# Kernel tuning notes

Measured on AMD Instinct MI355X. Metric: run time of the kernel, lower is better.

## Reference

```python
import jax, jax.numpy as jnp
from jax import lax
import numpy as np

B, T, IN, H, NC, NL = 128, 256, 64, 256, 1, 2


def _lstm_dir(x, w_ih, w_hh, b_ih, b_hh, reverse):
    """Single-direction LSTM over x:[B,T,in]. PyTorch gate order i,f,g,o."""
    Bd = x.shape[0]
    Hd = w_hh.shape[1]
    # precompute input contribution to gates: [T,B,4H]
    xg = jnp.einsum('bti,gi->tbg', x, w_ih) + b_ih + b_hh

    def step(carry, xg_t):
        h, c = carry
        g = xg_t + h @ w_hh.T                      # [B,4H]
        i, f, gg, o = jnp.split(g, 4, axis=-1)
        i = jax.nn.sigmoid(i)
        f = jax.nn.sigmoid(f)
        gg = jnp.tanh(gg)
        o = jax.nn.sigmoid(o)
        c = f * c + i * gg
        h = o * jnp.tanh(c)
        return (h, c), h

    h0 = jnp.zeros((Bd, Hd), x.dtype)
    _, hs = lax.scan(step, (h0, h0), xg, reverse=reverse)
    return jnp.swapaxes(hs, 0, 1)                  # [B,T,H], time-aligned


def _bilstm(x, params):
    out = x
    for l in range(NL):
        fwd = _lstm_dir(out, params[f'w_ih_l{l}f'], params[f'w_hh_l{l}f'],
                        params[f'b_ih_l{l}f'], params[f'b_hh_l{l}f'], reverse=False)
        bwd = _lstm_dir(out, params[f'w_ih_l{l}b'], params[f'w_hh_l{l}b'],
                        params[f'b_ih_l{l}b'], params[f'b_hh_l{l}b'], reverse=True)
        out = jnp.concatenate([fwd, bwd], axis=-1)  # [B,T,2H]
        # (nn.LSTM dropout=0.2 is train-only between layers; eval -> identity)
    return out


def setup_inputs() -> dict:
    key = jax.random.key(0)
    ks = iter(jax.random.split(key, 32))
    inp = {'x': jax.random.normal(next(ks), (B, T, IN), jnp.float32)}
    s = 1.0 / np.sqrt(H)
    for l in range(NL):
        isz = IN if l == 0 else 2 * H
        for d in ('f', 'b'):
            inp[f'w_ih_l{l}{d}'] = jax.random.uniform(next(ks), (4 * H, isz), jnp.float32, -s, s)
            inp[f'w_hh_l{l}{d}'] = jax.random.uniform(next(ks), (4 * H, H), jnp.float32, -s, s)
            inp[f'b_ih_l{l}{d}'] = jax.random.uniform(next(ks), (4 * H,), jnp.float32, -s, s)
            inp[f'b_hh_l{l}{d}'] = jax.random.uniform(next(ks), (4 * H,), jnp.float32, -s, s)
    inp['fc_w'] = jax.random.uniform(next(ks), (NC, 2 * H), jnp.float32, -s, s)
    inp['fc_b'] = jax.random.uniform(next(ks), (NC,), jnp.float32, -s, s)
    return inp


def reference(x,
              w_ih_l0f, w_hh_l0f, b_ih_l0f, b_hh_l0f,
              w_ih_l0b, w_hh_l0b, b_ih_l0b, b_hh_l0b,
              w_ih_l1f, w_hh_l1f, b_ih_l1f, b_hh_l1f,
              w_ih_l1b, w_hh_l1b, b_ih_l1b, b_hh_l1b,
              fc_w, fc_b):
    params = dict(w_ih_l0f=w_ih_l0f, w_hh_l0f=w_hh_l0f, b_ih_l0f=b_ih_l0f, b_hh_l0f=b_hh_l0f,
                  w_ih_l0b=w_ih_l0b, w_hh_l0b=w_hh_l0b, b_ih_l0b=b_ih_l0b, b_hh_l0b=b_hh_l0b,
                  w_ih_l1f=w_ih_l1f, w_hh_l1f=w_hh_l1f, b_ih_l1f=b_ih_l1f, b_hh_l1f=b_hh_l1f,
                  w_ih_l1b=w_ih_l1b, w_hh_l1b=w_hh_l1b, b_ih_l1b=b_ih_l1b, b_hh_l1b=b_hh_l1b)
    out = _bilstm(x, params)          # [B,T,2H]
    last = out[:, -1, :]              # [B,2H]
    return last @ fc_w.T + fc_b       # [B,NC]
```

## Files before the change

kernel.cpp:

```cpp
#include <hip/hip_runtime.h>


typedef unsigned long long ull;

constexpr int B_ = 128, T_ = 256, IN_ = 64, H_ = 256;
constexpr int JW = 64;

#define KEEP_REG(x) asm volatile("" : "+v"(x))

__device__ __forceinline__ float sigmoid_(float x) { return 1.f / (1.f + __expf(-x)); }
__device__ __forceinline__ float tanh_(float x)    { return 1.f - 2.f / (1.f + __expf(2.f * x)); }
__device__ __forceinline__ int hidx(int k) { return (k >> 6) * 68 + (k & 63); }
__device__ __forceinline__ int widx(int gp, int jl, int ks, int kp) {
  return ((gp * 64 + jl) * 4 + ks) * 68 + kp;
}

template<int BB, bool L0M>
__global__ __launch_bounds__(256, 1)
void recur(const float* __restrict__ whh_f, const float* __restrict__ whh_b,
           const float* __restrict__ wih_f, const float* __restrict__ wih_b,
           const float* __restrict__ bih_f, const float* __restrict__ bhh_f,
           const float* __restrict__ bih_b, const float* __restrict__ bhh_b,
           const float* __restrict__ x,
           const float* __restrict__ xg,
           float* __restrict__ out0,
           float* __restrict__ hstate, float* __restrict__ cstate,
           float* __restrict__ hfinal,
           ull* __restrict__ ring,
           int ngroup, int dir_base, int nsteps, int step_base,
           int first, int save, int lastW)
{
  const int bid = blockIdx.x;
  const int kw  = bid & 3;
  const int gr  = (bid >> 2) % ngroup;
  const int dl  = (bid >> 2) / ngroup;
  const int d   = dir_base + dl;
  const int tid = threadIdx.x;
  const int jl  = tid >> 2;
  const int ks  = tid & 3;
  const int j   = kw * JW + jl;
  const int bbase = gr * BB;
  const int gidx  = dl * ngroup + gr;

  const float* whh  = d ? whh_b : whh_f;
  const float* wihp = d ? wih_b : wih_f;

  float wr[2][64];
  #pragma unroll
  for (int g = 0; g < 2; ++g) {
    const float* wrow = whh + (long)(g * H_ + j) * H_ + ks * 64;
    #pragma unroll
    for (int q = 0; q < 16; ++q) {
      const float4 w4 = *(const float4*)(wrow + q * 4);
      wr[g][q*4+0] = w4.x; wr[g][q*4+1] = w4.y;
      wr[g][q*4+2] = w4.z; wr[g][q*4+3] = w4.w;
    }
  }
  #pragma unroll
  for (int g = 0; g < 2; ++g)
    #pragma unroll
    for (int q = 0; q < 64; ++q) KEEP_REG(wr[g][q]);

  __shared__ alignas(16) float wlds[2 * 64 * 4 * 68];
  __shared__ alignas(16) float hbuf[2][BB][272];
  __shared__ alignas(16) float xt[2][4][64];
  #pragma unroll
  for (int gp = 0; gp < 2; ++gp) {
    const float* wrow = whh + (long)((gp + 2) * H_ + j) * H_ + ks * 64;
    float* dst = &wlds[widx(gp, jl, ks, 0)];
    #pragma unroll
    for (int q = 0; q < 16; ++q)
      *(float4*)(dst + q * 4) = *(const float4*)(wrow + q * 4);
  }

  float br[4];
  if constexpr (L0M) {
    const float* bih = d ? bih_b : bih_f;
    const float* bhh = d ? bhh_b : bhh_f;
    #pragma unroll
    for (int g = 0; g < 4; ++g) br[g] = bih[g * H_ + j] + bhh[g * H_ + j];
  }

  for (int idx = tid; idx < BB * H_; idx += 256) {
    const int b = idx >> 8, k = idx & 255;
    hbuf[0][b][hidx(k)] = first ? 0.f : hstate[(long)(bbase + b) * H_ + k];
  }
  float cs[BB];
  #pragma unroll
  for (int b = 0; b < BB; ++b)
    cs[b] = first ? 0.f : cstate[(long)(bbase + b) * H_ + j];

  if constexpr (L0M) {
    const int b = tid >> 6, kx = tid & 63;
    const int t0 = d ? T_ - 1 : 0;
    xt[0][b][kx] = x[((long)(bbase + b) * T_ + t0) * IN_ + kx];
  }
  float xr[BB][4], xn[BB][4];
  if constexpr (!L0M) {
    #pragma unroll
    for (int b = 0; b < BB; ++b)
      #pragma unroll
      for (int g = 0; g < 4; ++g)
        xr[b][g] = xg[(long)(bbase + b) * 1024 + g * H_ + j];
  }
  __syncthreads();

  const long ringstride = (long)2 * BB * H_;

  for (int s = 0; s < nsteps; ++s) {
    const int p = s & 1, wp = p ^ 1;
    const int gstep = step_base + s;

    float xpre = 0.f;
    if constexpr (L0M) {
      if (s + 1 < nsteps) {
        const int b = tid >> 6, kx = tid & 63;
        const int ttn = d ? (T_ - 2 - s) : (s + 1);
        xpre = x[((long)(bbase + b) * T_ + ttn) * IN_ + kx];
      }
    } else {
      const int sn = (s + 1 < nsteps) ? s + 1 : s;
      #pragma unroll
      for (int b = 0; b < BB; ++b)
        #pragma unroll
        for (int g = 0; g < 4; ++g)
          xn[b][g] = xg[((long)sn * B_ + bbase + b) * 1024 + g * H_ + j];
    }

    float acc[BB][4];
    #pragma unroll
    for (int b = 0; b < BB; ++b)
      #pragma unroll
      for (int g = 0; g < 4; ++g) acc[b][g] = 0.f;

    if constexpr (L0M) {
      #pragma unroll
      for (int gp = 0; gp < 2; ++gp) {
        const int g0 = 2 * gp, g1 = 2 * gp + 1;
        const float* wa = wihp + (long)(g0 * H_ + j) * IN_ + ks * 16;
        const float* wb = wihp + (long)(g1 * H_ + j) * IN_ + ks * 16;
        float4 wa_[4], wb_[4];
        #pragma unroll
        for (int q = 0; q < 4; ++q) { wa_[q] = *(const float4*)(wa + q * 4);
                                      wb_[q] = *(const float4*)(wb + q * 4); }
        #pragma unroll
        for (int b = 0; b < BB; ++b) {
          #pragma unroll
          for (int q = 0; q < 4; ++q) {
            const float4 xv = *(const float4*)&xt[p][b][ks * 16 + q * 4];
            acc[b][g0] = fmaf(xv.x, wa_[q].x, acc[b][g0]);
            acc[b][g0] = fmaf(xv.y, wa_[q].y, acc[b][g0]);
            acc[b][g0] = fmaf(xv.z, wa_[q].z, acc[b][g0]);
            acc[b][g0] = fmaf(xv.w, wa_[q].w, acc[b][g0]);
            acc[b][g1] = fmaf(xv.x, wb_[q].x, acc[b][g1]);
            acc[b][g1] = fmaf(xv.y, wb_[q].y, acc[b][g1]);
            acc[b][g1] = fmaf(xv.z, wb_[q].z, acc[b][g1]);
            acc[b][g1] = fmaf(xv.w, wb_[q].w, acc[b][g1]);
          }
        }
      }
      if (s + 1 < nsteps) {
        const int b = tid >> 6, kx = tid & 63;
        xt[wp][b][kx] = xpre;
      }
    }

    if (s > 0) {
      const unsigned want = (unsigned)gstep;
      ull* rg = ring + gidx * ringstride + (long)((gstep - 1) & 1) * (BB * H_);
      constexpr int NP = 3 * JW * BB;
      constexpr int NL = (NP + 255) / 256;
      ull vv[NL];
      #pragma unroll
      for (int q = 0; q < NL; ++q) {
        const int pidx = tid + q * 256;
        if (pidx < NP) {
          const int psl = pidx / (JW * BB), rem = pidx % (JW * BB);
          const int kwp = psl + (psl >= kw ? 1 : 0);
          vv[q] = __hip_atomic_load(rg + (rem >> 6) * H_ + kwp * JW + (rem & 63),
                                    __ATOMIC_RELAXED, __HIP_MEMORY_SCOPE_AGENT);
        }
      }
      long gd = 0;
      for (;;) {
        bool ok = true;
        #pragma unroll
        for (int q = 0; q < NL; ++q)
          if (tid + q * 256 < NP && (unsigned)(vv[q] >> 32) != want) ok = false;
        if (ok) break;
        if (++gd > (1L << 20)) break;
        __builtin_amdgcn_s_sleep(1);
        #pragma unroll
        for (int q = 0; q < NL; ++q) {
          const int pidx = tid + q * 256;
          if (pidx < NP && (unsigned)(vv[q] >> 32) != want) {
            const int psl = pidx / (JW * BB), rem = pidx % (JW * BB);
            const int kwp = psl + (psl >= kw ? 1 : 0);
            vv[q] = __hip_atomic_load(rg + (rem >> 6) * H_ + kwp * JW + (rem & 63),
                                      __ATOMIC_RELAXED, __HIP_MEMORY_SCOPE_AGENT);
          }
        }
      }
      #pragma unroll
      for (int q = 0; q < NL; ++q) {
        const int pidx = tid + q * 256;
        if (pidx < NP) {
          const int psl = pidx / (JW * BB), rem = pidx % (JW * BB);
          const int kwp = psl + (psl >= kw ? 1 : 0);
          hbuf[p][rem >> 6][hidx(kwp * JW + (rem & 63))] =
              __uint_as_float((unsigned)vv[q]);
        }
      }
    }
    __syncthreads();

    #pragma unroll
    for (int q = 0; q < 16; ++q) {
      const float4 wg = *(const float4*)&wlds[widx(0, jl, ks, q * 4)];
      const float4 wo = *(const float4*)&wlds[widx(1, jl, ks, q * 4)];
      #pragma unroll
      for (int b = 0; b < BB; ++b) {
        const float4 hv = *(const float4*)&hbuf[p][b][ks * 68 + q * 4];
        acc[b][0] = fmaf(hv.x, wr[0][q*4+0], acc[b][0]);
        acc[b][0] = fmaf(hv.y, wr[0][q*4+1], acc[b][0]);
        acc[b][0] = fmaf(hv.z, wr[0][q*4+2], acc[b][0]);
        acc[b][0] = fmaf(hv.w, wr[0][q*4+3], acc[b][0]);
        acc[b][1] = fmaf(hv.x, wr[1][q*4+0], acc[b][1]);
        acc[b][1] = fmaf(hv.y, wr[1][q*4+1], acc[b][1]);
        acc[b][1] = fmaf(hv.z, wr[1][q*4+2], acc[b][1]);
        acc[b][1] = fmaf(hv.w, wr[1][q*4+3], acc[b][1]);
        acc[b][2] = fmaf(hv.x, wg.x, acc[b][2]);
        acc[b][2] = fmaf(hv.y, wg.y, acc[b][2]);
        acc[b][2] = fmaf(hv.z, wg.z, acc[b][2]);
        acc[b][2] = fmaf(hv.w, wg.w, acc[b][2]);
        acc[b][3] = fmaf(hv.x, wo.x, acc[b][3]);
        acc[b][3] = fmaf(hv.y, wo.y, acc[b][3]);
        acc[b][3] = fmaf(hv.z, wo.z, acc[b][3]);
        acc[b][3] = fmaf(hv.w, wo.w, acc[b][3]);
      }
    }

    float hv_[BB];
    #pragma unroll
    for (int b = 0; b < BB; ++b) {
      #pragma unroll
      for (int g = 0; g < 4; ++g) {
        float a = acc[b][g];
        a += __shfl_xor(a, 1, 64);
        a += __shfl_xor(a, 2, 64);
        if constexpr (L0M) acc[b][g] = a + br[g];
        else               acc[b][g] = a + xr[b][g];
      }
      const float ig = sigmoid_(acc[b][0]);
      const float fg = sigmoid_(acc[b][1]);
      const float gg = tanh_(acc[b][2]);
      const float og = sigmoid_(acc[b][3]);
      cs[b] = fg * cs[b] + ig * gg;
      hv_[b] = og * tanh_(cs[b]);
    }

    if (ks < BB) {
      float hmine = hv_[0], cmine = cs[0];
      #pragma unroll
      for (int b = 1; b < BB; ++b)
        if (ks == b) { hmine = hv_[b]; cmine = cs[b]; }

      if (s < nsteps - 1) {
        const ull pv = ((ull)(unsigned)(gstep + 1) << 32) | (unsigned)__float_as_uint(hmine);
        __hip_atomic_store(ring + gidx * ringstride + (long)(gstep & 1) * (BB * H_)
                               + ks * H_ + j,
                           pv, __ATOMIC_RELAXED, __HIP_MEMORY_SCOPE_AGENT);
      }
      hbuf[wp][ks][hidx(j)] = hmine;

      if constexpr (L0M) {
        const int tt = d ? (T_ - 1 - gstep) : gstep;
        out0[((long)tt * B_ + bbase + ks) * 512 + d * H_ + j] = hmine;
      } else {
        if (s == nsteps - 1 && lastW)
          hfinal[(long)(bbase + ks) * 512 + (d ? H_ : 0) + j] = hmine;
      }
      if (save && s == nsteps - 1) {
        hstate[(long)(bbase + ks) * H_ + j] = hmine;
        cstate[(long)(bbase + ks) * H_ + j] = cmine;
      }
    }

    if constexpr (!L0M) {
      #pragma unroll
      for (int b = 0; b < BB; ++b)
        #pragma unroll
        for (int g = 0; g < 4; ++g) xr[b][g] = xn[b][g];
    }
  }
}

__global__ __launch_bounds__(256, 2)
void xg_gemm(const float* __restrict__ A, const float* __restrict__ W,
             const float* __restrict__ b1, const float* __restrict__ b2,
             float* __restrict__ C)
{
  __shared__ float As[16][128];
  __shared__ float Bs[16][132];
  const int tid = threadIdx.x;
  const int tx = tid & 15, ty = tid >> 4;
  const long m0 = (long)blockIdx.x * 128;
  const int  n0 = blockIdx.y * 128;
  const int sr = tid >> 1;
  const int sk = (tid & 1) * 8;
  const float* Ar = A + (m0 + sr) * 512 + sk;
  const float* Wr = W + (long)(n0 + sr) * 512 + sk;
  float acc[8][8];
  #pragma unroll
  for (int i = 0; i < 8; ++i)
    #pragma unroll
    for (int jj = 0; jj < 8; ++jj) acc[i][jj] = 0.f;

// ... 56 lines not shown
  const float* wp = fc_w + q * 128;
  #pragma unroll 4
  for (int k = 0; k < 128; ++k) s += hp[k] * wp[k];
  s += __shfl_xor(s, 1, 64);
  s += __shfl_xor(s, 2, 64);
  if (q == 0) out[b] = s + fc_b[0];
}

extern "C" void kernel_launch(void* const* d_in, const int* in_sizes, int n_in,
                              void* d_out, int out_size, void* d_ws, size_t ws_size,
                              hipStream_t stream)
{
  const float* x     = (const float*)d_in[0];
  const float* wih0f = (const float*)d_in[1];
  const float* whh0f = (const float*)d_in[2];
  const float* bih0f = (const float*)d_in[3];
  const float* bhh0f = (const float*)d_in[4];
  const float* wih0b = (const float*)d_in[5];
  const float* whh0b = (const float*)d_in[6];
  const float* bih0b = (const float*)d_in[7];
  const float* bhh0b = (const float*)d_in[8];
  const float* wih1f = (const float*)d_in[9];
  const float* whh1f = (const float*)d_in[10];
  const float* bih1f = (const float*)d_in[11];
  const float* bhh1f = (const float*)d_in[12];
  const float* wih1b = (const float*)d_in[13];
  const float* whh1b = (const float*)d_in[14];
  const float* bih1b = (const float*)d_in[15];
  const float* bhh1b = (const float*)d_in[16];
  const float* fcw   = (const float*)d_in[17];
  const float* fcb   = (const float*)d_in[18];

  const size_t n_out0 = (size_t)T_ * B_ * 512;
  const size_t nring0 = 64ull * 2 * 4 * 256;
  const size_t nring1 = 64ull * 2 * 2 * 256;

  int CH = 0;
  const int cands[4] = {64, 32, 16, 8};
  const size_t fixedf = n_out0 + (size_t)B_ * 1024 + 2 * (size_t)B_ * 256
                      + (size_t)B_ * 512;
  for (int i = 0; i < 4; ++i) {
    const size_t need = 4 * (fixedf + (size_t)cands[i] * B_ * 1024)
                      + 8 * (nring0 + nring1);
    if (need <= ws_size) { CH = cands[i]; break; }
  }
  if (!CH) return;

  float* out0 = (float*)d_ws;
  float* xg1  = out0 + n_out0;
  float* xg1b = xg1 + (size_t)CH * B_ * 1024;
  float* hst1 = xg1b + (size_t)B_ * 1024;
  float* cst1 = hst1 + (size_t)B_ * 256;
  float* hfin = cst1 + (size_t)B_ * 256;
  ull*  ring0 = (ull*)(hfin + (size_t)B_ * 512);
  ull*  ring1 = ring0 + nring0;

  hipMemsetAsync(ring0, 0, (nring0 + nring1) * sizeof(ull), stream);

  recur<4, true><<<dim3(256), dim3(256), 0, stream>>>(
      whh0f, whh0b, wih0f, wih0b, bih0f, bhh0f, bih0b, bhh0b,
      x, nullptr, out0, nullptr, nullptr, nullptr, ring0,
      32, 0, T_, 0,
      1, 0, 0);

  xg_gemm<<<dim3(1, 8), dim3(256), 0, stream>>>(
      out0 + (size_t)(T_ - 1) * B_ * 512, wih1b, bih1b, bhh1b, xg1b);
  recur<2, false><<<dim3(256), dim3(256), 0, stream>>>(
      whh1f, whh1b, nullptr, nullptr, nullptr, nullptr, nullptr, nullptr,
      nullptr, xg1b, nullptr, hst1, cst1, hfin, ring1,
      64, 1, 1, 0,
      1, 0, 1);

  const int nch = T_ / CH;
  for (int c = 0; c < nch; ++c) {
    xg_gemm<<<dim3(CH, 8), dim3(256), 0, stream>>>(
        out0 + (size_t)c * CH * B_ * 512, wih1f, bih1f, bhh1f, xg1);
    recur<2, false><<<dim3(256), dim3(256), 0, stream>>>(
        whh1f, whh1b, nullptr, nullptr, nullptr, nullptr, nullptr, nullptr,
        nullptr, xg1, nullptr, hst1, cst1, hfin, ring1,
        64, 0, CH, c * CH,
        c == 0 ? 1 : 0, 1, c == nch - 1 ? 1 : 0);
  }

  fc_kernel<<<dim3(1), dim3(512), 0, stream>>>(hfin, fcw, fcb, (float*)d_out);
}
```

Measured before the change: 2.500 ms.

## Repartition LSTM recurrence into 512-thread block pairs with halved batch per block

Each batch group's hidden dimension is now split across 2 blocks of 512 threads instead of 4 blocks of 256, and each block handles half as many batch rows. Three gate weight slices stay in registers and the output gate moves to swizzled LDS. The cross-block ring exchange shrinks to one partner half, with a simpler per-thread spin wait. The host also launches the layer-1 input GEMM for all timesteps at once when the workspace is large enough. The aim is to cut inter-block synchronisation traffic and LDS weight reads per step. In exchange it raises register pressure at 512 threads and changes the xg_gemm grid shape.

```diff
diff --git a/kernel.cpp b/kernel.cpp
--- a/kernel.cpp
+++ b/kernel.cpp
@@ -4,19 +4,18 @@
 typedef unsigned long long ull;
 
 constexpr int B_ = 128, T_ = 256, IN_ = 64, H_ = 256;
-constexpr int JW = 64;
 
 #define KEEP_REG(x) asm volatile("" : "+v"(x))
 
 __device__ __forceinline__ float sigmoid_(float x) { return 1.f / (1.f + __expf(-x)); }
 __device__ __forceinline__ float tanh_(float x)    { return 1.f - 2.f / (1.f + __expf(2.f * x)); }
 __device__ __forceinline__ int hidx(int k) { return (k >> 6) * 68 + (k & 63); }
-__device__ __forceinline__ int widx(int gp, int jl, int ks, int kp) {
-  return ((gp * 64 + jl) * 4 + ks) * 68 + kp;
+__device__ __forceinline__ int oidx(int row, int kp) {
+  return row * 64 + (kp ^ ((row & 7) << 2));
 }
 
 template<int BB, bool L0M>
-__global__ __launch_bounds__(256, 1)
+__global__ __launch_bounds__(512, 1)
 void recur(const float* __restrict__ whh_f, const float* __restrict__ whh_b,
            const float* __restrict__ wih_f, const float* __restrict__ wih_b,
            const float* __restrict__ bih_f, const float* __restrict__ bhh_f,
@@ -30,24 +29,24 @@
            int ngroup, int dir_base, int nsteps, int step_base,
            int first, int save, int lastW)
 {
-  const int bid = blockIdx.x;
-  const int kw  = bid & 3;
-  const int gr  = (bid >> 2) % ngroup;
-  const int dl  = (bid >> 2) / ngroup;
-  const int d   = dir_base + dl;
-  const int tid = threadIdx.x;
-  const int jl  = tid >> 2;
-  const int ks  = tid & 3;
-  const int j   = kw * JW + jl;
+  const int bid  = blockIdx.x;
+  const int m    = bid & 1;
+  const int gidx = bid >> 1;
+  const int gr   = gidx % ngroup;
+  const int dl   = gidx / ngroup;
+  const int d    = dir_base + dl;
+  const int tid  = threadIdx.x;
+  const int jl   = tid >> 2;
+  const int ks   = tid & 3;
+  const int j    = m * 128 + jl;
   const int bbase = gr * BB;
-  const int gidx  = dl * ngroup + gr;
 
   const float* whh  = d ? whh_b : whh_f;
   const float* wihp = d ? wih_b : wih_f;
 
-  float wr[2][64];
-  #pragma unroll
-  for (int g = 0; g < 2; ++g) {
+  float wr[3][64];
+  #pragma unroll
+  for (int g = 0; g < 3; ++g) {
     const float* wrow = whh + (long)(g * H_ + j) * H_ + ks * 64;
     #pragma unroll
     for (int q = 0; q < 16; ++q) {
@@ -57,20 +56,18 @@
     }
   }
   #pragma unroll
-  for (int g = 0; g < 2; ++g)
+  for (int g = 0; g < 3; ++g)
     #pragma unroll
     for (int q = 0; q < 64; ++q) KEEP_REG(wr[g][q]);
 
-  __shared__ alignas(16) float wlds[2 * 64 * 4 * 68];
+  __shared__ alignas(16) float wo_lds[512 * 64];
   __shared__ alignas(16) float hbuf[2][BB][272];
-  __shared__ alignas(16) float xt[2][4][64];
-  #pragma unroll
-  for (int gp = 0; gp < 2; ++gp) {
-    const float* wrow = whh + (long)((gp + 2) * H_ + j) * H_ + ks * 64;
-    float* dst = &wlds[widx(gp, jl, ks, 0)];
-    #pragma unroll
-    for (int q = 0; q < 16; ++q)
-      *(float4*)(dst + q * 4) = *(const float4*)(wrow + q * 4);
+  __shared__ alignas(16) float xt[2][BB][64];
+  {
+    const float* wrow = whh + (long)(3 * H_ + j) * H_ + ks * 64;
+    #pragma unroll
+    for (int s = 0; s < 16; ++s)
+      *(float4*)&wo_lds[oidx(tid, s * 4)] = *(const float4*)(wrow + s * 4);
   }
 
   float br[4];
@@ -81,7 +78,7 @@
     for (int g = 0; g < 4; ++g) br[g] = bih[g * H_ + j] + bhh[g * H_ + j];
   }
 
-  for (int idx = tid; idx < BB * H_; idx += 256) {
+  for (int idx = tid; idx < BB * H_; idx += 512) {
     const int b = idx >> 8, k = idx & 255;
     hbuf[0][b][hidx(k)] = first ? 0.f : hstate[(long)(bbase + b) * H_ + k];
   }
@@ -91,9 +88,11 @@
     cs[b] = first ? 0.f : cstate[(long)(bbase + b) * H_ + j];
 
   if constexpr (L0M) {
-    const int b = tid >> 6, kx = tid & 63;
-    const int t0 = d ? T_ - 1 : 0;
-    xt[0][b][kx] = x[((long)(bbase + b) * T_ + t0) * IN_ + kx];
+    if (tid < BB * 64) {
+      const int b = tid >> 6, kx = tid & 63;
+      const int t0 = d ? T_ - 1 : 0;
+      xt[0][b][kx] = x[((long)(bbase + b) * T_ + t0) * IN_ + kx];
+    }
   }
   float xr[BB][4], xn[BB][4];
   if constexpr (!L0M) {
@@ -105,7 +104,7 @@
   }
   __syncthreads();
 
-  const long ringstride = (long)2 * BB * H_;
+  const long RS = (long)2 * BB * 256;
 
   for (int s = 0; s < nsteps; ++s) {
     const int p = s & 1, wp = p ^ 1;
@@ -113,7 +112,7 @@
 
     float xpre = 0.f;
     if constexpr (L0M) {
-      if (s + 1 < nsteps) {
+      if (s + 1 < nsteps && tid < BB * 64) {
         const int b = tid >> 6, kx = tid & 63;
         const int ttn = d ? (T_ - 2 - s) : (s + 1);
         xpre = x[((long)(bbase + b) * T_ + ttn) * IN_ + kx];
@@ -135,89 +134,52 @@
 
     if constexpr (L0M) {
       #pragma unroll
-      for (int gp = 0; gp < 2; ++gp) {
-        const int g0 = 2 * gp, g1 = 2 * gp + 1;
-        const float* wa = wihp + (long)(g0 * H_ + j) * IN_ + ks * 16;
-        const float* wb = wihp + (long)(g1 * H_ + j) * IN_ + ks * 16;
-        float4 wa_[4], wb_[4];
+      for (int g = 0; g < 4; ++g) {
+        const float* wa = wihp + (long)(g * H_ + j) * IN_ + ks * 16;
+        float4 w_[4];
         #pragma unroll
-        for (int q = 0; q < 4; ++q) { wa_[q] = *(const float4*)(wa + q * 4);
-                                      wb_[q] = *(const float4*)(wb + q * 4); }
+        for (int q = 0; q < 4; ++q) w_[q] = *(const float4*)(wa + q * 4);
         #pragma unroll
         for (int b = 0; b < BB; ++b) {
           #pragma unroll
           for (int q = 0; q < 4; ++q) {
             const float4 xv = *(const float4*)&xt[p][b][ks * 16 + q * 4];
-            acc[b][g0] = fmaf(xv.x, wa_[q].x, acc[b][g0]);
-            acc[b][g0] = fmaf(xv.y, wa_[q].y, acc[b][g0]);
-            acc[b][g0] = fmaf(xv.z, wa_[q].z, acc[b][g0]);
-            acc[b][g0] = fmaf(xv.w, wa_[q].w, acc[b][g0]);
-            acc[b][g1] = fmaf(xv.x, wb_[q].x, acc[b][g1]);
-            acc[b][g1] = fmaf(xv.y, wb_[q].y, acc[b][g1]);
-            acc[b][g1] = fmaf(xv.z, wb_[q].z, acc[b][g1]);
-            acc[b][g1] = fmaf(xv.w, wb_[q].w, acc[b][g1]);
+            acc[b][g] = fmaf(xv.x, w_[q].x, acc[b][g]);
+            acc[b][g] = fmaf(xv.y, w_[q].y, acc[b][g]);
+            acc[b][g] = fmaf(xv.z, w_[q].z, acc[b][g]);
+            acc[b][g] = fmaf(xv.w, w_[q].w, acc[b][g]);
           }
         }
       }
-      if (s + 1 < nsteps) {
+      if (s + 1 < nsteps && tid < BB * 64) {
         const int b = tid >> 6, kx = tid & 63;
         xt[wp][b][kx] = xpre;
       }
     }
 
     if (s > 0) {
-      const unsigned want = (unsigned)gstep;
-      ull* rg = ring + gidx * ringstride + (long)((gstep - 1) & 1) * (BB * H_);
-      constexpr int NP = 3 * JW * BB;
-      constexpr int NL = (NP + 255) / 256;
-      ull vv[NL];
-      #pragma unroll
-      for (int q = 0; q < NL; ++q) {
-        const int pidx = tid + q * 256;
-        if (pidx < NP) {
-          const int psl = pidx / (JW * BB), rem = pidx % (JW * BB);
-          const int kwp = psl + (psl >= kw ? 1 : 0);
-          vv[q] = __hip_atomic_load(rg + (rem >> 6) * H_ + kwp * JW + (rem & 63),
-                                    __ATOMIC_RELAXED, __HIP_MEMORY_SCOPE_AGENT);
+      constexpr int NP = BB * 128;
+      if (tid < NP) {
+        const unsigned want = (unsigned)gstep;
+        const int b  = tid >> 7;
+        const int pj = (1 - m) * 128 + (tid & 127);
+        const ull* addr = ring + gidx * RS
+                        + (long)((gstep - 1) & 1) * (BB * 256) + b * 256 + pj;
+        ull v = __hip_atomic_load(addr, __ATOMIC_RELAXED, __HIP_MEMORY_SCOPE_AGENT);
+        long gd = 0;
+        while ((unsigned)(v >> 32) != want) {
+          __builtin_amdgcn_s_sleep(1);
+          if (++gd > (1L << 20)) break;
+          v = __hip_atomic_load(addr, __ATOMIC_RELAXED, __HIP_MEMORY_SCOPE_AGENT);
         }
-      }
-      long gd = 0;
-      for (;;) {
-        bool ok = true;
-        #pragma unroll
-        for (int q = 0; q < NL; ++q)
-          if (tid + q * 256 < NP && (unsigned)(vv[q] >> 32) != want) ok = false;
-        if (ok) break;
-        if (++gd > (1L << 20)) break;
-        __builtin_amdgcn_s_sleep(1);
-        #pragma unroll
-        for (int q = 0; q < NL; ++q) {
-          const int pidx = tid + q * 256;
-          if (pidx < NP && (unsigned)(vv[q] >> 32) != want) {
-            const int psl = pidx / (JW * BB), rem = pidx % (JW * BB);
-            const int kwp = psl + (psl >= kw ? 1 : 0);
-            vv[q] = __hip_atomic_load(rg + (rem >> 6) * H_ + kwp * JW + (rem & 63),
-                                      __ATOMIC_RELAXED, __HIP_MEMORY_SCOPE_AGENT);
-          }
-        }
-      }
-      #pragma unroll
-      for (int q = 0; q < NL; ++q) {
-        const int pidx = tid + q * 256;
-        if (pidx < NP) {
-          const int psl = pidx / (JW * BB), rem = pidx % (JW * BB);
-          const int kwp = psl + (psl >= kw ? 1 : 0);
-          hbuf[p][rem >> 6][hidx(kwp * JW + (rem & 63))] =
-              __uint_as_float((unsigned)vv[q]);
-        }
+        hbuf[p][b][hidx(pj)] = __uint_as_float((unsigned)v);
       }
     }
     __syncthreads();
 
     #pragma unroll
     for (int q = 0; q < 16; ++q) {
-      const float4 wg = *(const float4*)&wlds[widx(0, jl, ks, q * 4)];
-      const float4 wo = *(const float4*)&wlds[widx(1, jl, ks, q * 4)];
+      const float4 wo = *(const float4*)&wo_lds[oidx(tid, q * 4)];
       #pragma unroll
       for (int b = 0; b < BB; ++b) {
         const float4 hv = *(const float4*)&hbuf[p][b][ks * 68 + q * 4];
@@ -229,10 +191,10 @@
         acc[b][1] = fmaf(hv.y, wr[1][q*4+1], acc[b][1]);
         acc[b][1] = fmaf(hv.z, wr[1][q*4+2], acc[b][1]);
         acc[b][1] = fmaf(hv.w, wr[1][q*4+3], acc[b][1]);
-        acc[b][2] = fmaf(hv.x, wg.x, acc[b][2]);
-        acc[b][2] = fmaf(hv.y, wg.y, acc[b][2]);
-        acc[b][2] = fmaf(hv.z, wg.z, acc[b][2]);
-        acc[b][2] = fmaf(hv.w, wg.w, acc[b][2]);
+        acc[b][2] = fmaf(hv.x, wr[2][q*4+0], acc[b][2]);
+        acc[b][2] = fmaf(hv.y, wr[2][q*4+1], acc[b][2]);
+        acc[b][2] = fmaf(hv.z, wr[2][q*4+2], acc[b][2]);
+        acc[b][2] = fmaf(hv.w, wr[2][q*4+3], acc[b][2]);
         acc[b][3] = fmaf(hv.x, wo.x, acc[b][3]);
         acc[b][3] = fmaf(hv.y, wo.y, acc[b][3]);
         acc[b][3] = fmaf(hv.z, wo.z, acc[b][3]);
@@ -266,9 +228,10 @@
         if (ks == b) { hmine = hv_[b]; cmine = cs[b]; }
 
       if (s < nsteps - 1) {
-        const ull pv = ((ull)(unsigned)(gstep + 1) << 32) | (unsigned)__float_as_uint(hmine);
-        __hip_atomic_store(ring + gidx * ringstride + (long)(gstep & 1) * (BB * H_)
-                               + ks * H_ + j,
+        const ull pv = ((ull)(unsigned)(gstep + 1) << 32)
+                     | (unsigned)__float_as_uint(hmine);
+        __hip_atomic_store(ring + gidx * RS + (long)(gstep & 1) * (BB * 256)
+                               + ks * 256 + j,
                            pv, __ATOMIC_RELAXED, __HIP_MEMORY_SCOPE_AGENT);
       }
       hbuf[wp][ks][hidx(j)] = hmine;
@@ -405,54 +368,70 @@
   const float* fcb   = (const float*)d_in[18];
 
   const size_t n_out0 = (size_t)T_ * B_ * 512;
-  const size_t nring0 = 64ull * 2 * 4 * 256;
-  const size_t nring1 = 64ull * 2 * 2 * 256;
-
-  int CH = 0;
-  const int cands[4] = {64, 32, 16, 8};
-  const size_t fixedf = n_out0 + (size_t)B_ * 1024 + 2 * (size_t)B_ * 256
-                      + (size_t)B_ * 512;
-  for (int i = 0; i < 4; ++i) {
-    const size_t need = 4 * (fixedf + (size_t)cands[i] * B_ * 1024)
-                      + 8 * (nring0 + nring1);
-    if (need <= ws_size) { CH = cands[i]; break; }
+  const size_t n_xg1b = (size_t)B_ * 1024;
+  const size_t n_hst  = (size_t)B_ * 256;
+  const size_t n_hfin = (size_t)B_ * 512;
+  const size_t nring0 = 128ull * 2 * 2 * 256;
+  const size_t nring1 = 128ull * 2 * 1 * 256;
+  const size_t fixedf = n_out0 + n_xg1b + 2 * n_hst + n_hfin;
+  const size_t ringB  = (nring0 + nring1) * sizeof(ull);
+
+  int CH = 0; bool full = false;
+  if (4 * (fixedf + (size_t)T_ * B_ * 1024) + ringB <= ws_size) {
+    full = true; CH = T_;
+  } else {
+    const int cands[4] = {64, 32, 16, 8};
+    for (int i = 0; i < 4; ++i)
+      if (4 * (fixedf + (size_t)cands[i] * B_ * 1024) + ringB <= ws_size) {
+        CH = cands[i]; break;
+      }
   }
   if (!CH) return;
 
   float* out0 = (float*)d_ws;
-  float* xg1  = out0 + n_out0;
-  float* xg1b = xg1 + (size_t)CH * B_ * 1024;
-  float* hst1 = xg1b + (size_t)B_ * 1024;
-  float* cst1 = hst1 + (size_t)B_ * 256;
-  float* hfin = cst1 + (size_t)B_ * 256;
-  ull*  ring0 = (ull*)(hfin + (size_t)B_ * 512);
+  float* xga  = out0 + n_out0;
+  float* xg1b = xga + (size_t)CH * B_ * 1024;
+  float* hst1 = xg1b + n_xg1b;
+  float* cst1 = hst1 + n_hst;
+  float* hfin = cst1 + n_hst;
+  ull*  ring0 = (ull*)(hfin + n_hfin);
   ull*  ring1 = ring0 + nring0;
 
-  hipMemsetAsync(ring0, 0, (nring0 + nring1) * sizeof(ull), stream);
-
-  recur<4, true><<<dim3(256), dim3(256), 0, stream>>>(
+  hipMemsetAsync(ring0, 0, ringB, stream);
+
+  recur<2, true><<<dim3(256), dim3(512), 0, stream>>>(
       whh0f, whh0b, wih0f, wih0b, bih0f, bhh0f, bih0b, bhh0b,
       x, nullptr, out0, nullptr, nullptr, nullptr, ring0,
-      32, 0, T_, 0,
+      64, 0, T_, 0,
       1, 0, 0);
 
   xg_gemm<<<dim3(1, 8), dim3(256), 0, stream>>>(
       out0 + (size_t)(T_ - 1) * B_ * 512, wih1b, bih1b, bhh1b, xg1b);
-  recur<2, false><<<dim3(256), dim3(256), 0, stream>>>(
+  recur<1, false><<<dim3(256), dim3(512), 0, stream>>>(
       whh1f, whh1b, nullptr, nullptr, nullptr, nullptr, nullptr, nullptr,
       nullptr, xg1b, nullptr, hst1, cst1, hfin, ring1,
-      64, 1, 1, 0,
+      128, 1, 1, 0,
       1, 0, 1);
 
-  const int nch = T_ / CH;
-  for (int c = 0; c < nch; ++c) {
-    xg_gemm<<<dim3(CH, 8), dim3(256), 0, stream>>>(
-        out0 + (size_t)c * CH * B_ * 512, wih1f, bih1f, bhh1f, xg1);
-    recur<2, false><<<dim3(256), dim3(256), 0, stream>>>(
+  if (full) {
+    xg_gemm<<<dim3(T_ * B_ / 128, 8), dim3(256), 0, stream>>>(
+        out0, wih1f, bih1f, bhh1f, xga);
+    recur<1, false><<<dim3(256), dim3(512), 0, stream>>>(
         whh1f, whh1b, nullptr, nullptr, nullptr, nullptr, nullptr, nullptr,
-        nullptr, xg1, nullptr, hst1, cst1, hfin, ring1,
-        64, 0, CH, c * CH,
-        c == 0 ? 1 : 0, 1, c == nch - 1 ? 1 : 0);
+        nullptr, xga, nullptr, hst1, cst1, hfin, ring1,
+        128, 0, T_, 0,
+        1, 0, 1);
+  } else {
+    const int nch = T_ / CH;
+    for (int c = 0; c < nch; ++c) {
+      xg_gemm<<<dim3(CH * B_ / 128, 8), dim3(256), 0, stream>>>(
+          out0 + (size_t)c * CH * B_ * 512, wih1f, bih1f, bhh1f, xga);
+      recur<1, false><<<dim3(256), dim3(512), 0, stream>>>(
+          whh1f, whh1b, nullptr, nullptr, nullptr, nullptr, nullptr, nullptr,
+          nullptr, xga, nullptr, hst1, cst1, hfin, ring1,
+          128, 0, CH, c * CH,
+          c == 0 ? 1 : 0, 1, c == nch - 1 ? 1 : 0);
+    }
   }
 
   fc_kernel<<<dim3(1), dim3(512), 0, stream>>>(hfin, fcw, fcb, (float*)d_out);
```

After: 3.211 ms. +28.4%, slower.

## Pipeline recurrent step per batch row and run layer-1 forward in one launch

Applied to the files above, without the earlier changes.

The recurrent kernel now waits for, computes and publishes each batch row's hidden state one at a time, instead of waiting for all rows before any matmul. A row's result can be sent to peer blocks while later rows are still computing, which shortens the cross-block dependency chain. On the host, when the workspace is large enough, the layer-1 input-gate GEMM runs over all timesteps in one launch, followed by a single recurrent launch, replacing the chunked loop. The trade-off is more __syncthreads per step (one per row) and a larger workspace; the xg_gemm grid sizing also changes from CH to CH*B/128.

```diff
diff --git a/kernel.cpp b/kernel.cpp
--- a/kernel.cpp
+++ b/kernel.cpp
@@ -91,9 +91,11 @@
     cs[b] = first ? 0.f : cstate[(long)(bbase + b) * H_ + j];
 
   if constexpr (L0M) {
-    const int b = tid >> 6, kx = tid & 63;
-    const int t0 = d ? T_ - 1 : 0;
-    xt[0][b][kx] = x[((long)(bbase + b) * T_ + t0) * IN_ + kx];
+    if (tid < BB * 64) {
+      const int b = tid >> 6, kx = tid & 63;
+      const int t0 = d ? T_ - 1 : 0;
+      xt[0][b][kx] = x[((long)(bbase + b) * T_ + t0) * IN_ + kx];
+    }
   }
   float xr[BB][4], xn[BB][4];
   if constexpr (!L0M) {
@@ -113,7 +115,7 @@
 
     float xpre = 0.f;
     if constexpr (L0M) {
-      if (s + 1 < nsteps) {
+      if (s + 1 < nsteps && tid < BB * 64) {
         const int b = tid >> 6, kx = tid & 63;
         const int ttn = d ? (T_ - 2 - s) : (s + 1);
         xpre = x[((long)(bbase + b) * T_ + ttn) * IN_ + kx];
@@ -159,130 +161,89 @@
           }
         }
       }
-      if (s + 1 < nsteps) {
+      if (s + 1 < nsteps && tid < BB * 64) {
         const int b = tid >> 6, kx = tid & 63;
         xt[wp][b][kx] = xpre;
       }
     }
 
-    if (s > 0) {
-      const unsigned want = (unsigned)gstep;
-      ull* rg = ring + gidx * ringstride + (long)((gstep - 1) & 1) * (BB * H_);
-      constexpr int NP = 3 * JW * BB;
-      constexpr int NL = (NP + 255) / 256;
-      ull vv[NL];
-      #pragma unroll
-      for (int q = 0; q < NL; ++q) {
-        const int pidx = tid + q * 256;
-        if (pidx < NP) {
-          const int psl = pidx / (JW * BB), rem = pidx % (JW * BB);
-          const int kwp = psl + (psl >= kw ? 1 : 0);
-          vv[q] = __hip_atomic_load(rg + (rem >> 6) * H_ + kwp * JW + (rem & 63),
-                                    __ATOMIC_RELAXED, __HIP_MEMORY_SCOPE_AGENT);
+    #pragma unroll
+    for (int st = 0; st < BB; ++st) {
+      if (s > 0 && tid < 3 * JW) {
+        const unsigned want = (unsigned)gstep;
+        const int psl = tid / JW;
+        const int kwp = psl + (psl >= kw ? 1 : 0);
+        const int jp  = kwp * JW + (tid % JW);
+        const ull* addr = ring + gidx * ringstride
+                        + (long)((gstep - 1) & 1) * (BB * H_) + st * H_ + jp;
+        ull v = __hip_atomic_load(addr, __ATOMIC_RELAXED, __HIP_MEMORY_SCOPE_AGENT);
+        long gd = 0;
+        while ((unsigned)(v >> 32) != want) {
+          __builtin_amdgcn_s_sleep(1);
+          if (++gd > (1L << 20)) break;
+          v = __hip_atomic_load(addr, __ATOMIC_RELAXED, __HIP_MEMORY_SCOPE_AGENT);
         }
-      }
-      long gd = 0;
-      for (;;) {
-        bool ok = true;
-        #pragma unroll
-        for (int q = 0; q < NL; ++q)
-          if (tid + q * 256 < NP && (unsigned)(vv[q] >> 32) != want) ok = false;
-        if (ok) break;
-        if (++gd > (1L << 20)) break;
-        __builtin_amdgcn_s_sleep(1);
-        #pragma unroll
-        for (int q = 0; q < NL; ++q) {
-          const int pidx = tid + q * 256;
-          if (pidx < NP && (unsigned)(vv[q] >> 32) != want) {
-            const int psl = pidx / (JW * BB), rem = pidx % (JW * BB);
-            const int kwp = psl + (psl >= kw ? 1 : 0);
-            vv[q] = __hip_atomic_load(rg + (rem >> 6) * H_ + kwp * JW + (rem & 63),
-                                      __ATOMIC_RELAXED, __HIP_MEMORY_SCOPE_AGENT);
-          }
+        hbuf[p][st][hidx(jp)] = __uint_as_float((unsigned)v);
+      }
+      __syncthreads();
+
+      float a0 = acc[st][0], a1 = acc[st][1], a2 = acc[st][2], a3 = acc[st][3];
+      #pragma unroll
+      for (int q = 0; q < 16; ++q) {
+        const float4 wg = *(const float4*)&wlds[widx(0, jl, ks, q * 4)];
+        const float4 wo = *(const float4*)&wlds[widx(1, jl, ks, q * 4)];
+        const float4 hv = *(const float4*)&hbuf[p][st][ks * 68 + q * 4];
+        a0 = fmaf(hv.x, wr[0][q*4+0], a0);
+        a0 = fmaf(hv.y, wr[0][q*4+1], a0);
+        a0 = fmaf(hv.z, wr[0][q*4+2], a0);
+        a0 = fmaf(hv.w, wr[0][q*4+3], a0);
+        a1 = fmaf(hv.x, wr[1][q*4+0], a1);
+        a1 = fmaf(hv.y, wr[1][q*4+1], a1);
+        a1 = fmaf(hv.z, wr[1][q*4+2], a1);
+        a1 = fmaf(hv.w, wr[1][q*4+3], a1);
+        a2 = fmaf(hv.x, wg.x, a2);
+        a2 = fmaf(hv.y, wg.y, a2);
+        a2 = fmaf(hv.z, wg.z, a2);
+        a2 = fmaf(hv.w, wg.w, a2);
+        a3 = fmaf(hv.x, wo.x, a3);
+        a3 = fmaf(hv.y, wo.y, a3);
+        a3 = fmaf(hv.z, wo.z, a3);
+        a3 = fmaf(hv.w, wo.w, a3);
+      }
+
+      a0 += __shfl_xor(a0, 1, 64); a0 += __shfl_xor(a0, 2, 64);
+      a1 += __shfl_xor(a1, 1, 64); a1 += __shfl_xor(a1, 2, 64);
+      a2 += __shfl_xor(a2, 1, 64); a2 += __shfl_xor(a2, 2, 64);
+      a3 += __shfl_xor(a3, 1, 64); a3 += __shfl_xor(a3, 2, 64);
+      if constexpr (L0M) { a0 += br[0]; a1 += br[1]; a2 += br[2]; a3 += br[3]; }
+      else { a0 += xr[st][0]; a1 += xr[st][1]; a2 += xr[st][2]; a3 += xr[st][3]; }
+      const float ig = sigmoid_(a0);
+      const float fg = sigmoid_(a1);
+      const float gg = tanh_(a2);
+      const float og = sigmoid_(a3);
+      cs[st] = fg * cs[st] + ig * gg;
+      const float hv_ = og * tanh_(cs[st]);
+
+      if (ks == 0) {
+        if (s < nsteps - 1) {
+          const ull pv = ((ull)(unsigned)(gstep + 1) << 32)
+                       | (unsigned)__float_as_uint(hv_);
+          __hip_atomic_store(ring + gidx * ringstride
+                                 + (long)(gstep & 1) * (BB * H_) + st * H_ + j,
+                             pv, __ATOMIC_RELAXED, __HIP_MEMORY_SCOPE_AGENT);
         }
-      }
-      #pragma unroll
-      for (int q = 0; q < NL; ++q) {
-        const int pidx = tid + q * 256;
-        if (pidx < NP) {
-          const int psl = pidx / (JW * BB), rem = pidx % (JW * BB);
-          const int kwp = psl + (psl >= kw ? 1 : 0);
-          hbuf[p][rem >> 6][hidx(kwp * JW + (rem & 63))] =
-              __uint_as_float((unsigned)vv[q]);
+        hbuf[wp][st][hidx(j)] = hv_;
+        if constexpr (L0M) {
+          const int tt = d ? (T_ - 1 - gstep) : gstep;
+          out0[((long)tt * B_ + bbase + st) * 512 + d * H_ + j] = hv_;
+        } else {
+          if (s == nsteps - 1 && lastW)
+            hfinal[(long)(bbase + st) * 512 + (d ? H_ : 0) + j] = hv_;
         }
-      }
-    }
-    __syncthreads();
-
-    #pragma unroll
-    for (int q = 0; q < 16; ++q) {
-      const float4 wg = *(const float4*)&wlds[widx(0, jl, ks, q * 4)];
-      const float4 wo = *(const float4*)&wlds[widx(1, jl, ks, q * 4)];
-      #pragma unroll
-      for (int b = 0; b < BB; ++b) {
-        const float4 hv = *(const float4*)&hbuf[p][b][ks * 68 + q * 4];
-        acc[b][0] = fmaf(hv.x, wr[0][q*4+0], acc[b][0]);
-        acc[b][0] = fmaf(hv.y, wr[0][q*4+1], acc[b][0]);
-        acc[b][0] = fmaf(hv.z, wr[0][q*4+2], acc[b][0]);
-        acc[b][0] = fmaf(hv.w, wr[0][q*4+3], acc[b][0]);
-        acc[b][1] = fmaf(hv.x, wr[1][q*4+0], acc[b][1]);
-        acc[b][1] = fmaf(hv.y, wr[1][q*4+1], acc[b][1]);
-        acc[b][1] = fmaf(hv.z, wr[1][q*4+2], acc[b][1]);
-        acc[b][1] = fmaf(hv.w, wr[1][q*4+3], acc[b][1]);
-        acc[b][2] = fmaf(hv.x, wg.x, acc[b][2]);
-        acc[b][2] = fmaf(hv.y, wg.y, acc[b][2]);
-        acc[b][2] = fmaf(hv.z, wg.z, acc[b][2]);
-        acc[b][2] = fmaf(hv.w, wg.w, acc[b][2]);
-        acc[b][3] = fmaf(hv.x, wo.x, acc[b][3]);
-        acc[b][3] = fmaf(hv.y, wo.y, acc[b][3]);
-        acc[b][3] = fmaf(hv.z, wo.z, acc[b][3]);
-        acc[b][3] = fmaf(hv.w, wo.w, acc[b][3]);
-      }
-    }
-
-    float hv_[BB];
-    #pragma unroll
-    for (int b = 0; b < BB; ++b) {
-      #pragma unroll
-      for (int g = 0; g < 4; ++g) {
-        float a = acc[b][g];
-        a += __shfl_xor(a, 1, 64);
-        a += __shfl_xor(a, 2, 64);
-        if constexpr (L0M) acc[b][g] = a + br[g];
-        else               acc[b][g] = a + xr[b][g];
-      }
-      const float ig = sigmoid_(acc[b][0]);
-      const float fg = sigmoid_(acc[b][1]);
-      const float gg = tanh_(acc[b][2]);
-      const float og = sigmoid_(acc[b][3]);
-      cs[b] = fg * cs[b] + ig * gg;
-      hv_[b] = og * tanh_(cs[b]);
-    }
-
-    if (ks < BB) {
-      float hmine = hv_[0], cmine = cs[0];
-      #pragma unroll
-      for (int b = 1; b < BB; ++b)
-        if (ks == b) { hmine = hv_[b]; cmine = cs[b]; }
-
-      if (s < nsteps - 1) {
-        const ull pv = ((ull)(unsigned)(gstep + 1) << 32) | (unsigned)__float_as_uint(hmine);
-        __hip_atomic_store(ring + gidx * ringstride + (long)(gstep & 1) * (BB * H_)
-                               + ks * H_ + j,
-                           pv, __ATOMIC_RELAXED, __HIP_MEMORY_SCOPE_AGENT);
-      }
-      hbuf[wp][ks][hidx(j)] = hmine;
-
-      if constexpr (L0M) {
-        const int tt = d ? (T_ - 1 - gstep) : gstep;
-        out0[((long)tt * B_ + bbase + ks) * 512 + d * H_ + j] = hmine;
-      } else {
-        if (s == nsteps - 1 && lastW)
-          hfinal[(long)(bbase + ks) * 512 + (d ? H_ : 0) + j] = hmine;
-      }
-      if (save && s == nsteps - 1) {
-        hstate[(long)(bbase + ks) * H_ + j] = hmine;
-        cstate[(long)(bbase + ks) * H_ + j] = cmine;
+        if (save && s == nsteps - 1) {
+          hstate[(long)(bbase + st) * H_ + j] = hv_;
+          cstate[(long)(bbase + st) * H_ + j] = cs[st];
+        }
       }
     }
 
@@ -407,28 +368,32 @@
   const size_t n_out0 = (size_t)T_ * B_ * 512;
   const size_t nring0 = 64ull * 2 * 4 * 256;
   const size_t nring1 = 64ull * 2 * 2 * 256;
-
-  int CH = 0;
-  const int cands[4] = {64, 32, 16, 8};
+  const size_t ringB  = (nring0 + nring1) * sizeof(ull);
   const size_t fixedf = n_out0 + (size_t)B_ * 1024 + 2 * (size_t)B_ * 256
                       + (size_t)B_ * 512;
-  for (int i = 0; i < 4; ++i) {
-    const size_t need = 4 * (fixedf + (size_t)cands[i] * B_ * 1024)
-                      + 8 * (nring0 + nring1);
-    if (need <= ws_size) { CH = cands[i]; break; }
+
+  int CH = 0; bool full = false;
+  if (4 * (fixedf + (size_t)T_ * B_ * 1024) + ringB <= ws_size) {
+    full = true; CH = T_;
+  } else {
+    const int cands[4] = {64, 32, 16, 8};
+    for (int i = 0; i < 4; ++i)
+      if (4 * (fixedf + (size_t)cands[i] * B_ * 1024) + ringB <= ws_size) {
+        CH = cands[i]; break;
+      }
   }
   if (!CH) return;
 
   float* out0 = (float*)d_ws;
-  float* xg1  = out0 + n_out0;
-  float* xg1b = xg1 + (size_t)CH * B_ * 1024;
+  float* xga  = out0 + n_out0;
+  float* xg1b = xga + (size_t)CH * B_ * 1024;
   float* hst1 = xg1b + (size_t)B_ * 1024;
   float* cst1 = hst1 + (size_t)B_ * 256;
   float* hfin = cst1 + (size_t)B_ * 256;
   ull*  ring0 = (ull*)(hfin + (size_t)B_ * 512);
   ull*  ring1 = ring0 + nring0;
 
-  hipMemsetAsync(ring0, 0, (nring0 + nring1) * sizeof(ull), stream);
+  hipMemsetAsync(ring0, 0, ringB, stream);
 
   recur<4, true><<<dim3(256), dim3(256), 0, stream>>>(
       whh0f, whh0b, wih0f, wih0b, bih0f, bhh0f, bih0b, bhh0b,
@@ -444,15 +409,25 @@
       64, 1, 1, 0,
       1, 0, 1);
 
-  const int nch = T_ / CH;
-  for (int c = 0; c < nch; ++c) {
-    xg_gemm<<<dim3(CH, 8), dim3(256), 0, stream>>>(
-        out0 + (size_t)c * CH * B_ * 512, wih1f, bih1f, bhh1f, xg1);
+  if (full) {
+    xg_gemm<<<dim3(T_ * B_ / 128, 8), dim3(256), 0, stream>>>(
+        out0, wih1f, bih1f, bhh1f, xga);
     recur<2, false><<<dim3(256), dim3(256), 0, stream>>>(
         whh1f, whh1b, nullptr, nullptr, nullptr, nullptr, nullptr, nullptr,
-        nullptr, xg1, nullptr, hst1, cst1, hfin, ring1,
-        64, 0, CH, c * CH,
-        c == 0 ? 1 : 0, 1, c == nch - 1 ? 1 : 0);
+        nullptr, xga, nullptr, hst1, cst1, hfin, ring1,
+        64, 0, T_, 0,
+        1, 0, 1);
+  } else {
+    const int nch = T_ / CH;
+    for (int c = 0; c < nch; ++c) {
+      xg_gemm<<<dim3(CH * B_ / 128, 8), dim3(256), 0, stream>>>(
+          out0 + (size_t)c * CH * B_ * 512, wih1f, bih1f, bhh1f, xga);
+      recur<2, false><<<dim3(256), dim3(256), 0, stream>>>(
+          whh1f, whh1b, nullptr, nullptr, nullptr, nullptr, nullptr, nullptr,
+          nullptr, xga, nullptr, hst1, cst1, hfin, ring1,
+          64, 0, CH, c * CH,
+          c == 0 ? 1 : 0, 1, c == nch - 1 ? 1 : 0);
+    }
   }
 
   fc_kernel<<<dim3(1), dim3(512), 0, stream>>>(hfin, fcw, fcb, (float*)d_out);
```

Result: slower. 3.213 ms (+28.5%).

## Issue ring loads before input projection and run layer-1 unchunked when workspace allows

Applied to the files above, without the earlier changes.

In the recurrent kernel, the relaxed atomic loads of neighbour hidden states from the ring are now issued before the layer-0 input-projection FMAs, and the W_ih weights are loaded at the top of the step. The aim is to hide cross-block communication latency behind that compute. On the host side, if the workspace can hold the full [T,B,4H] gate precompute, layer 1 runs as a single GEMM plus a single recurrent launch instead of a chunked loop, which removes repeated launches and the state save/restore between chunks. The changes cost extra registers for prefetched values and need a much larger workspace.

```diff
diff --git a/kernel.cpp b/kernel.cpp
--- a/kernel.cpp
+++ b/kernel.cpp
@@ -91,9 +91,11 @@
     cs[b] = first ? 0.f : cstate[(long)(bbase + b) * H_ + j];
 
   if constexpr (L0M) {
-    const int b = tid >> 6, kx = tid & 63;
-    const int t0 = d ? T_ - 1 : 0;
-    xt[0][b][kx] = x[((long)(bbase + b) * T_ + t0) * IN_ + kx];
+    if (tid < BB * 64) {
+      const int b = tid >> 6, kx = tid & 63;
+      const int t0 = d ? T_ - 1 : 0;
+      xt[0][b][kx] = x[((long)(bbase + b) * T_ + t0) * IN_ + kx];
+    }
   }
   float xr[BB][4], xn[BB][4];
   if constexpr (!L0M) {
@@ -106,14 +108,30 @@
   __syncthreads();
 
   const long ringstride = (long)2 * BB * H_;
+  constexpr int NP = 3 * JW * BB;
+  constexpr int NL = (NP + 255) / 256;
 
   for (int s = 0; s < nsteps; ++s) {
     const int p = s & 1, wp = p ^ 1;
     const int gstep = step_base + s;
 
+    float4 wa_[2][4], wb_[2][4];
+    if constexpr (L0M) {
+      #pragma unroll
+      for (int gp = 0; gp < 2; ++gp) {
+        const float* wa = wihp + (long)((2 * gp) * H_ + j) * IN_ + ks * 16;
+        const float* wb = wihp + (long)((2 * gp + 1) * H_ + j) * IN_ + ks * 16;
+        #pragma unroll
+        for (int q = 0; q < 4; ++q) {
+          wa_[gp][q] = *(const float4*)(wa + q * 4);
+          wb_[gp][q] = *(const float4*)(wb + q * 4);
+        }
+      }
+    }
+
     float xpre = 0.f;
     if constexpr (L0M) {
-      if (s + 1 < nsteps) {
+      if (s + 1 < nsteps && tid < BB * 64) {
         const int b = tid >> 6, kx = tid & 63;
         const int ttn = d ? (T_ - 2 - s) : (s + 1);
         xpre = x[((long)(bbase + b) * T_ + ttn) * IN_ + kx];
@@ -127,60 +145,57 @@
           xn[b][g] = xg[((long)sn * B_ + bbase + b) * 1024 + g * H_ + j];
     }
 
-    float acc[BB][4];
-    #pragma unroll
-    for (int b = 0; b < BB; ++b)
-      #pragma unroll
-      for (int g = 0; g < 4; ++g) acc[b][g] = 0.f;
-
-    if constexpr (L0M) {
-      #pragma unroll
-      for (int gp = 0; gp < 2; ++gp) {
-        const int g0 = 2 * gp, g1 = 2 * gp + 1;
-        const float* wa = wihp + (long)(g0 * H_ + j) * IN_ + ks * 16;
-        const float* wb = wihp + (long)(g1 * H_ + j) * IN_ + ks * 16;
-        float4 wa_[4], wb_[4];
-        #pragma unroll
-        for (int q = 0; q < 4; ++q) { wa_[q] = *(const float4*)(wa + q * 4);
-                                      wb_[q] = *(const float4*)(wb + q * 4); }
-        #pragma unroll
-        for (int b = 0; b < BB; ++b) {
-          #pragma unroll
-          for (int q = 0; q < 4; ++q) {
-            const float4 xv = *(const float4*)&xt[p][b][ks * 16 + q * 4];
-            acc[b][g0] = fmaf(xv.x, wa_[q].x, acc[b][g0]);
-            acc[b][g0] = fmaf(xv.y, wa_[q].y, acc[b][g0]);
-            acc[b][g0] = fmaf(xv.z, wa_[q].z, acc[b][g0]);
-            acc[b][g0] = fmaf(xv.w, wa_[q].w, acc[b][g0]);
-            acc[b][g1] = fmaf(xv.x, wb_[q].x, acc[b][g1]);
-            acc[b][g1] = fmaf(xv.y, wb_[q].y, acc[b][g1]);
-            acc[b][g1] = fmaf(xv.z, wb_[q].z, acc[b][g1]);
-            acc[b][g1] = fmaf(xv.w, wb_[q].w, acc[b][g1]);
-          }
-        }
-      }
-      if (s + 1 < nsteps) {
-        const int b = tid >> 6, kx = tid & 63;
-        xt[wp][b][kx] = xpre;
-      }
-    }
-
+    ull vv[NL];
     if (s > 0) {
-      const unsigned want = (unsigned)gstep;
-      ull* rg = ring + gidx * ringstride + (long)((gstep - 1) & 1) * (BB * H_);
-      constexpr int NP = 3 * JW * BB;
-      constexpr int NL = (NP + 255) / 256;
-      ull vv[NL];
+      const long roff = gidx * ringstride + (long)((gstep - 1) & 1) * (BB * H_);
       #pragma unroll
       for (int q = 0; q < NL; ++q) {
         const int pidx = tid + q * 256;
         if (pidx < NP) {
           const int psl = pidx / (JW * BB), rem = pidx % (JW * BB);
           const int kwp = psl + (psl >= kw ? 1 : 0);
-          vv[q] = __hip_atomic_load(rg + (rem >> 6) * H_ + kwp * JW + (rem & 63),
+          vv[q] = __hip_atomic_load(ring + roff + (rem >> 6) * H_
+                                        + kwp * JW + (rem & 63),
                                     __ATOMIC_RELAXED, __HIP_MEMORY_SCOPE_AGENT);
         }
       }
+    }
+
+    float acc[BB][4];
+    #pragma unroll
+    for (int b = 0; b < BB; ++b)
+      #pragma unroll
+      for (int g = 0; g < 4; ++g) acc[b][g] = 0.f;
+
+    if constexpr (L0M) {
+      #pragma unroll
+      for (int gp = 0; gp < 2; ++gp) {
+        const int g0 = 2 * gp, g1 = 2 * gp + 1;
+        #pragma unroll
+        for (int b = 0; b < BB; ++b) {
+          #pragma unroll
+          for (int q = 0; q < 4; ++q) {
+            const float4 xv = *(const float4*)&xt[p][b][ks * 16 + q * 4];
+            acc[b][g0] = fmaf(xv.x, wa_[gp][q].x, acc[b][g0]);
+            acc[b][g0] = fmaf(xv.y, wa_[gp][q].y, acc[b][g0]);
+            acc[b][g0] = fmaf(xv.z, wa_[gp][q].z, acc[b][g0]);
+            acc[b][g0] = fmaf(xv.w, wa_[gp][q].w, acc[b][g0]);
+            acc[b][g1] = fmaf(xv.x, wb_[gp][q].x, acc[b][g1]);
+            acc[b][g1] = fmaf(xv.y, wb_[gp][q].y, acc[b][g1]);
+            acc[b][g1] = fmaf(xv.z, wb_[gp][q].z, acc[b][g1]);
+            acc[b][g1] = fmaf(xv.w, wb_[gp][q].w, acc[b][g1]);
+          }
+        }
+      }
+      if (s + 1 < nsteps && tid < BB * 64) {
+        const int b = tid >> 6, kx = tid & 63;
+        xt[wp][b][kx] = xpre;
+      }
+    }
+
+    if (s > 0) {
+      const unsigned want = (unsigned)gstep;
+      const long roff = gidx * ringstride + (long)((gstep - 1) & 1) * (BB * H_);
       long gd = 0;
       for (;;) {
         bool ok = true;
@@ -196,7 +211,8 @@
           if (pidx < NP && (unsigned)(vv[q] >> 32) != want) {
             const int psl = pidx / (JW * BB), rem = pidx % (JW * BB);
             const int kwp = psl + (psl >= kw ? 1 : 0);
-            vv[q] = __hip_atomic_load(rg + (rem >> 6) * H_ + kwp * JW + (rem & 63),
+            vv[q] = __hip_atomic_load(ring + roff + (rem >> 6) * H_
+                                          + kwp * JW + (rem & 63),
                                       __ATOMIC_RELAXED, __HIP_MEMORY_SCOPE_AGENT);
           }
         }
@@ -266,9 +282,10 @@
         if (ks == b) { hmine = hv_[b]; cmine = cs[b]; }
 
       if (s < nsteps - 1) {
-        const ull pv = ((ull)(unsigned)(gstep + 1) << 32) | (unsigned)__float_as_uint(hmine);
-        __hip_atomic_store(ring + gidx * ringstride + (long)(gstep & 1) * (BB * H_)
-                               + ks * H_ + j,
+        const ull pv = ((ull)(unsigned)(gstep + 1) << 32)
+                     | (unsigned)__float_as_uint(hmine);
+        __hip_atomic_store(ring + gidx * ringstride
+                               + (long)(gstep & 1) * (BB * H_) + ks * H_ + j,
                            pv, __ATOMIC_RELAXED, __HIP_MEMORY_SCOPE_AGENT);
       }
       hbuf[wp][ks][hidx(j)] = hmine;
@@ -407,28 +424,32 @@
   const size_t n_out0 = (size_t)T_ * B_ * 512;
   const size_t nring0 = 64ull * 2 * 4 * 256;
   const size_t nring1 = 64ull * 2 * 2 * 256;
-
-  int CH = 0;
-  const int cands[4] = {64, 32, 16, 8};
+  const size_t ringB  = (nring0 + nring1) * sizeof(ull);
   const size_t fixedf = n_out0 + (size_t)B_ * 1024 + 2 * (size_t)B_ * 256
                       + (size_t)B_ * 512;
-  for (int i = 0; i < 4; ++i) {
-    const size_t need = 4 * (fixedf + (size_t)cands[i] * B_ * 1024)
-                      + 8 * (nring0 + nring1);
-    if (need <= ws_size) { CH = cands[i]; break; }
+
+  int CH = 0; bool full = false;
+  if (4 * (fixedf + (size_t)T_ * B_ * 1024) + ringB <= ws_size) {
+    full = true; CH = T_;
+  } else {
+    const int cands[4] = {64, 32, 16, 8};
+    for (int i = 0; i < 4; ++i)
+      if (4 * (fixedf + (size_t)cands[i] * B_ * 1024) + ringB <= ws_size) {
+        CH = cands[i]; break;
+      }
   }
   if (!CH) return;
 
   float* out0 = (float*)d_ws;
-  float* xg1  = out0 + n_out0;
-  float* xg1b = xg1 + (size_t)CH * B_ * 1024;
+  float* xga  = out0 + n_out0;
+  float* xg1b = xga + (size_t)CH * B_ * 1024;
   float* hst1 = xg1b + (size_t)B_ * 1024;
   float* cst1 = hst1 + (size_t)B_ * 256;
   float* hfin = cst1 + (size_t)B_ * 256;
   ull*  ring0 = (ull*)(hfin + (size_t)B_ * 512);
   ull*  ring1 = ring0 + nring0;
 
-  hipMemsetAsync(ring0, 0, (nring0 + nring1) * sizeof(ull), stream);
+  hipMemsetAsync(ring0, 0, ringB, stream);
 
   recur<4, true><<<dim3(256), dim3(256), 0, stream>>>(
       whh0f, whh0b, wih0f, wih0b, bih0f, bhh0f, bih0b, bhh0b,
@@ -444,15 +465,25 @@
       64, 1, 1, 0,
       1, 0, 1);
 
-  const int nch = T_ / CH;
-  for (int c = 0; c < nch; ++c) {
-    xg_gemm<<<dim3(CH, 8), dim3(256), 0, stream>>>(
-        out0 + (size_t)c * CH * B_ * 512, wih1f, bih1f, bhh1f, xg1);
+  if (full) {
+    xg_gemm<<<dim3(T_ * B_ / 128, 8), dim3(256), 0, stream>>>(
+        out0, wih1f, bih1f, bhh1f, xga);
     recur<2, false><<<dim3(256), dim3(256), 0, stream>>>(
         whh1f, whh1b, nullptr, nullptr, nullptr, nullptr, nullptr, nullptr,
-        nullptr, xg1, nullptr, hst1, cst1, hfin, ring1,
-        64, 0, CH, c * CH,
-        c == 0 ? 1 : 0, 1, c == nch - 1 ? 1 : 0);
+        nullptr, xga, nullptr, hst1, cst1, hfin, ring1,
+        64, 0, T_, 0,
+        1, 0, 1);
+  } else {
+    const int nch = T_ / CH;
+    for (int c = 0; c < nch; ++c) {
+      xg_gemm<<<dim3(CH * B_ / 128, 8), dim3(256), 0, stream>>>(
+          out0 + (size_t)c * CH * B_ * 512, wih1f, bih1f, bhh1f, xga);
+      recur<2, false><<<dim3(256), dim3(256), 0, stream>>>(
+          whh1f, whh1b, nullptr, nullptr, nullptr, nullptr, nullptr, nullptr,
+          nullptr, xga, nullptr, hst1, cst1, hfin, ring1,
+          64, 0, CH, c * CH,
+          c == 0 ? 1 : 0, 1, c == nch - 1 ? 1 : 0);
+    }
   }
 
   fc_kernel<<<dim3(1), dim3(512), 0, stream>>>(hfin, fcw, fcb, (float*)d_out);
```

Result: slower. 2.566 ms (+2.6%).
